# Performance work log

Hardware: AMD Instinct MI355X
Metric: run time of the kernel (lower is better)

## Reference

```python
import jax, jax.numpy as jnp
import numpy as np

N = 8192      # num nodes (pad index == N, matching the original's 15004 sentinel)
IN = 128; H = 128; OUT = 128
T = 512       # number of teams
L = 30        # max_len
SAMPLE = 5    # sample team size
DCAT = 2 * H + OUT


def _glorot(k, shape):
    lim = np.sqrt(6.0 / (shape[0] + shape[1]))
    return jax.random.uniform(k, shape, jnp.float32, -lim, lim)


def setup_inputs() -> dict:
    key = jax.random.key(0)
    ks = jax.random.split(key, 32)
    x = jax.random.normal(ks[0], (1, N, IN), jnp.float32)
    # sparse-ish binary dense adjacency, avg degree ~16 (memory-bound adj@x)
    adj = (jax.random.uniform(ks[1], (1, N, N), jnp.float32) < 16.0 / N).astype(jnp.float32)
    # team index matrix, ragged lengths in [SAMPLE+1, L], padded with N
    lens = jax.random.randint(ks[2], (T,), SAMPLE + 1, L + 1)
    ids = jax.random.randint(ks[3], (T, L), 0, N)
    teams = jnp.where(jnp.arange(L)[None, :] < lens[:, None], ids, N)
    # DenseGraphConv params: lin_rel (W,b) on adj@x, lin_root (no bias) on x
    p = dict(
        W1r=_glorot(ks[4], (IN, H)), b1=jnp.zeros((H,), jnp.float32), W1s=_glorot(ks[5], (IN, H)),
        W2r=_glorot(ks[6], (H, H)), b2=jnp.zeros((H,), jnp.float32), W2s=_glorot(ks[7], (H, H)),
        W3r=_glorot(ks[8], (H, OUT)), b3=jnp.zeros((OUT,), jnp.float32), W3s=_glorot(ks[9], (H, OUT)),
        g1=jnp.ones((H,), jnp.float32), be1=jnp.zeros((H,), jnp.float32),
        g2=jnp.ones((H,), jnp.float32), be2=jnp.zeros((H,), jnp.float32),
        g3=jnp.ones((OUT,), jnp.float32), be3=jnp.zeros((OUT,), jnp.float32),
        Wl=_glorot(ks[10], (DCAT, OUT)), bl=jnp.zeros((OUT,), jnp.float32),
        att=_glorot(ks[11], (T, L)),  # xavier_uniform'd attention vectors
    )
    return dict(x=x, adj=adj, teams=teams, sample_len=SAMPLE, **p)


def _bn(h, g, b):
    # BatchNorm1d in training mode over flattened (B*N, C), biased variance
    B, n, C = h.shape
    h2 = h.reshape(-1, C)
    mu = h2.mean(0)
    var = h2.var(0)
    return (((h2 - mu) * jax.lax.rsqrt(var + 1e-5)) * g + b).reshape(B, n, C)


def _conv(x, adj, Wr, br, Ws):
    # DenseGraphConv: lin_rel(adj @ x) + lin_root(x)
    return jnp.einsum('bnm,bmf,fo->bno', adj, x, Wr) + br + jnp.einsum('bnf,fo->bno', x, Ws)


def reference(x, adj, teams, sample_len, W1r, b1, W1s, W2r, b2, W2s, W3r, b3, W3s,
              g1, be1, g2, be2, g3, be3, Wl, bl, att):
    x1 = _bn(jax.nn.relu(_conv(x, adj, W1r, b1, W1s)), g1, be1)
    x2 = _bn(jax.nn.relu(_conv(x1, adj, W2r, b2, W2s)), g2, be2)
    x3 = _bn(jax.nn.relu(_conv(x2, adj, W3r, b3, W3s)), g3, be3)
    xcat = jnp.concatenate([x1, x2, x3], axis=-1)               # [1,N,DCAT]
    s = jax.nn.relu(xcat @ Wl + bl)
    appended = jnp.concatenate([xcat[0], jnp.zeros((1, xcat.shape[-1]), xcat.dtype)], 0)  # [N+1,D]
    gathered = appended[teams]                                   # [T,L,D] ragged gather
    # team: full softmax over attention vector (pad positions keep softmax mass,
    # but gather the zero row -> contribute zero, matching the original)
    a_team = jax.nn.softmax(att, axis=-1)
    team_emb = jnp.einsum('tl,tld->td', a_team, gathered)
    pos = jnp.arange(teams.shape[1])[None, :]
    # sample: sub-softmax over the attention entries at the sample members' positions
    m_s = pos < sample_len
    a_s = jax.nn.softmax(jnp.where(m_s, att, -1e30), axis=-1)
    sample_emb = jnp.einsum('tl,tld->td', a_s, gathered)
    # remain: team minus sample minus pad sentinel
    m_r = (pos >= sample_len) & (teams != N)
    a_r = jax.nn.softmax(jnp.where(m_r, att, -1e30), axis=-1)
    remain_emb = jnp.einsum('tl,tld->td', a_r, gathered)
    return s, xcat, team_emb, sample_emb, remain_emb
```

## Files before the change

### kernel.cpp

```cpp
#include <hip/hip_runtime.h>
#include <stdint.h>

#define NN 8192
#define CC 128
#define TT 512
#define LL 30
#define CAP 64

typedef unsigned int uint32;
typedef unsigned short u16;

typedef float f32x4 __attribute__((ext_vector_type(4)));
typedef short bf16x8 __attribute__((ext_vector_type(8)));

__device__ __forceinline__ float bf2f(uint32 h) { return __uint_as_float(h << 16); }
__device__ __forceinline__ u16 f2bf(float f) {
    uint32 u = __float_as_uint(f);
    u = (u + 0x7fffu + ((u >> 16) & 1u)) >> 16;
    return (u16)u;
}
__device__ __forceinline__ uint32 pack2(float a, float b) {
    return (uint32)f2bf(a) | ((uint32)f2bf(b) << 16);
}

__device__ __forceinline__ void stats_reduce(const float* __restrict__ P,
                                             const float* __restrict__ g,
                                             const float* __restrict__ be,
                                             float* __restrict__ coefOut, int tid) {
    __shared__ float SS[256], QQ[256];
    int c = tid & 127, half = tid >> 7;
    float s = 0.f, q = 0.f;
    int b0 = half * 128;
#pragma unroll 8
    for (int b = b0; b < b0 + 128; ++b) {
        s += P[b * 256 + c];
        q += P[b * 256 + 128 + c];
    }
    SS[tid] = s; QQ[tid] = q;
    __syncthreads();
    if (tid < 128) {
        float sum = SS[tid] + SS[tid + 128];
        float sq = QQ[tid] + QQ[tid + 128];
        float mu = sum * (1.f / NN);
        float var = sq * (1.f / NN) - mu * mu;
        float rs = rsqrtf(var + 1e-5f);
        float a = g[tid] * rs;
        coefOut[tid] = a;
        coefOut[128 + tid] = be[tid] - mu * a;
    }
}

__global__ __launch_bounds__(256) void k_pre(
    const float* __restrict__ adj,
    const float* __restrict__ W1r, const float* __restrict__ W1s,
    const float* __restrict__ W2r, const float* __restrict__ W2s,
    const float* __restrict__ W3r, const float* __restrict__ W3s,
    const float* __restrict__ Wl, const float* __restrict__ x0,
    int* __restrict__ nbr, int* __restrict__ cnt,
    u16* __restrict__ wfrag, u16* __restrict__ x0bf,
    u16* __restrict__ yp1, u16* __restrict__ yp2, u16* __restrict__ yp3,
    float* __restrict__ coefs) {
    int b = blockIdx.x, tid = threadIdx.x;
    if (b < 2048) {
        int row = b * 4 + (tid >> 6);
        int lane = tid & 63;
        const float4* arow = (const float4*)(adj + (size_t)row * NN);
        int base = 0;
        int* dst = nbr + (size_t)row * CAP;
        for (int it = 0; it < 32; ++it) {
            float4 v = arow[it * 64 + lane];
            float vv[4] = {v.x, v.y, v.z, v.w};
#pragma unroll
            for (int j = 0; j < 4; ++j) {
                unsigned long long m = __ballot(vv[j] != 0.f);
                if (vv[j] != 0.f) {
                    int pos = base + __popcll(m & ((1ull << lane) - 1ull));
                    if (pos < CAP) dst[pos] = it * 256 + lane * 4 + j;
                }
                base += __popcll(m);
            }
        }
        int nn = base < CAP ? base : CAP;
        int npad = (nn + 3) & ~3;
        for (int p = nn + lane; p < npad; p += 64) dst[p] = NN;
        if (lane == 0) cnt[row] = nn;
    } else if (b < 2336) {
        int bb = b - 2048;
        const float* Wa;
        const float* Wb;
        int tile, gbase;
        if (bb < 64)       { Wa = W1r; Wb = W1s; tile = bb;       gbase = 0; }
        else if (bb < 128) { Wa = W2r; Wb = W2s; tile = bb - 64;  gbase = 64; }
        else if (bb < 192) { Wa = W3r; Wb = W3s; tile = bb - 128; gbase = 128; }
        else               { Wa = Wl;  Wb = nullptr; tile = bb - 192; gbase = 192; }
        int kt = tile >> 3, nt = tile & 7;
        int lane = tid & 63, i0 = (tid >> 6) * 2;
        int n = nt * 16 + (lane & 15);
        u16* dst = wfrag + ((size_t)(gbase + tile) * 64 + lane) * 8;
#pragma unroll
        for (int ii = 0; ii < 2; ++ii) {
            int i = i0 + ii;
            int k = kt * 32 + ((lane >> 4) * 8) + i;
            float v;
            if (Wb) v = (k < 128) ? Wa[k * CC + n] : Wb[(k - 128) * CC + n];
            else    v = Wa[k * CC + n];
            dst[i] = f2bf(v);
        }
    } else if (b < 3360) {
        int idx = (b - 2336) * 1024 + tid * 4;
        float4 v = *(const float4*)(x0 + idx);
        ushort4 o;
        o.x = f2bf(v.x); o.y = f2bf(v.y); o.z = f2bf(v.z); o.w = f2bf(v.w);
        *(ushort4*)(x0bf + idx) = o;
    } else {
        if (tid < 128) {
            x0bf[(size_t)NN * CC + tid] = 0;
            yp1[(size_t)NN * CC + tid] = 0;
            yp2[(size_t)NN * CC + tid] = 0;
            yp3[(size_t)NN * CC + tid] = 0;
            coefs[tid] = 1.f;
            coefs[128 + tid] = 0.f;
        }
    }
}

__global__ __launch_bounds__(256) void k_agg(const u16* __restrict__ src,
                                             const int* __restrict__ nbr,
                                             const int* __restrict__ cnt,
                                             u16* __restrict__ Abraw,
                                             const float* __restrict__ P,
                                             const float* __restrict__ g,
                                             const float* __restrict__ be,
                                             float* __restrict__ coefOut) {
    if (blockIdx.x >= 2048) {
        stats_reduce(P, g, be, coefOut, threadIdx.x);
        return;
    }
    int row = blockIdx.x * 4 + (threadIdx.x >> 6);
    int lane = threadIdx.x & 63;
    int c = lane * 2;
    int nreal = cnt[row];
    int npad = (nreal + 3) & ~3;
    const int* nb = nbr + (size_t)row * CAP;
    float a0 = 0.f, a1 = 0.f;
    for (int j = 0; j < npad; j += 4) {
        int4 m = *(const int4*)(nb + j);
        uint32 v0 = *(const uint32*)(src + (size_t)m.x * CC + c);
        uint32 v1 = *(const uint32*)(src + (size_t)m.y * CC + c);
        uint32 v2 = *(const uint32*)(src + (size_t)m.z * CC + c);
        uint32 v3 = *(const uint32*)(src + (size_t)m.w * CC + c);
        a0 += bf2f(v0 & 0xffffu); a1 += bf2f(v0 >> 16);
        a0 += bf2f(v1 & 0xffffu); a1 += bf2f(v1 >> 16);
        a0 += bf2f(v2 & 0xffffu); a1 += bf2f(v2 >> 16);
        a0 += bf2f(v3 & 0xffffu); a1 += bf2f(v3 >> 16);
    }
    *(uint32*)(Abraw + (size_t)row * CC + c) = pack2(a0, a1);
}

__global__ __launch_bounds__(256) void k_gemm(const u16* __restrict__ Abraw,
                                              const u16* __restrict__ yprev,
                                              const int* __restrict__ cnt,
                                              const u16* __restrict__ wfrag,
                                              const float* __restrict__ bias,
                                              const float* __restrict__ coefIn,
                                              u16* __restrict__ yp,
                                              float* __restrict__ partials) {
    __shared__ u16 A[32][264];
    __shared__ float sSum[CC], sSq[CC];
    int tid = threadIdx.x, lane = tid & 63, wid = tid >> 6;
    int row0 = blockIdx.x * 32;
    if (tid < CC) { sSum[tid] = 0.f; sSq[tid] = 0.f; }
    for (int i = tid; i < 1024; i += 256) {
        int r = i >> 5, k = (i & 31) * 8;
        int row = row0 + r;
        uint4 raw;
        float fn;
        int c;
        if (k < 128) {
            c = k;
            raw = *(const uint4*)(Abraw + (size_t)row * CC + k);
            fn = (float)cnt[row];
        } else {
            c = k - 128;
            raw = *(const uint4*)(yprev + (size_t)row * CC + c);
            fn = 1.f;
        }
        float4 a0 = *(const float4*)(coefIn + c);
        float4 a1 = *(const float4*)(coefIn + c + 4);
        float4 b0 = *(const float4*)(coefIn + 128 + c);
        float4 b1 = *(const float4*)(coefIn + 128 + c + 4);
        uint4 o;
        o.x = pack2(a0.x * bf2f(raw.x & 0xffffu) + b0.x * fn, a0.y * bf2f(raw.x >> 16) + b0.y * fn);
        o.y = pack2(a0.z * bf2f(raw.y & 0xffffu) + b0.z * fn, a0.w * bf2f(raw.y >> 16) + b0.w * fn);
        o.z = pack2(a1.x * bf2f(raw.z & 0xffffu) + b1.x * fn, a1.y * bf2f(raw.z >> 16) + b1.y * fn);
        o.w = pack2(a1.z * bf2f(raw.w & 0xffffu) + b1.z * fn, a1.w * bf2f(raw.w >> 16) + b1.w * fn);
        *(uint4*)&A[r][k] = o;
    }
    __syncthreads();

    int mh = wid >> 1, nh = wid & 1;
    int arow = mh * 16 + (lane & 15);
    int kg = (lane >> 4) * 8;
    f32x4 acc[4];
#pragma unroll
    for (int nt = 0; nt < 4; ++nt) acc[nt] = (f32x4){0.f, 0.f, 0.f, 0.f};
#pragma unroll
    for (int kt = 0; kt < 8; ++kt) {
        bf16x8 a = *(const bf16x8*)&A[arow][kt * 32 + kg];
        const u16* wb = wfrag + ((size_t)(kt * 8 + nh * 4) * 64 + lane) * 8;
#pragma unroll
        for (int nt = 0; nt < 4; ++nt) {
            bf16x8 bfr = *(const bf16x8*)(wb + (size_t)nt * 512);
            acc[nt] = __builtin_amdgcn_mfma_f32_16x16x32_bf16(a, bfr, acc[nt], 0, 0, 0);
        }
    }
    int rowb = row0 + mh * 16 + ((lane >> 4) * 4);
#pragma unroll
    for (int nt = 0; nt < 4; ++nt) {
        int col = nh * 64 + nt * 16 + (lane & 15);
        float bv = bias[col];
        float s1 = 0.f, s2 = 0.f;
#pragma unroll
        for (int q = 0; q < 4; ++q) {
            float y = acc[nt][q] + bv;
            y = y > 0.f ? y : 0.f;
            yp[(size_t)(rowb + q) * CC + col] = f2bf(y);
            s1 += y;
            s2 += y * y;
        }
        s1 += __shfl_xor(s1, 16); s1 += __shfl_xor(s1, 32);
        s2 += __shfl_xor(s2, 16); s2 += __shfl_xor(s2, 32);
        if ((lane >> 4) == 0) { atomicAdd(&sSum[col], s1); atomicAdd(&sSq[col], s2); }
    }
    __syncthreads();
    if (tid < CC) {
        partials[(size_t)blockIdx.x * 256 + tid] = sSum[tid];
        partials[(size_t)blockIdx.x * 256 + CC + tid] = sSq[tid];
    }
}

__global__ __launch_bounds__(256) void k_coef3(const float* __restrict__ P,
                                               const float* __restrict__ g,
                                               const float* __restrict__ be,
                                               float* __restrict__ coefOut) {
    stats_reduce(P, g, be, coefOut, threadIdx.x);
}

__global__ __launch_bounds__(256) void k_gfinal(const u16* __restrict__ yp1,
                                                const u16* __restrict__ yp2,
                                                const u16* __restrict__ yp3,
                                                const float* __restrict__ coefs,
                                                const u16* __restrict__ wfrag,
                                                const float* __restrict__ bias,
                                                float* __restrict__ sout) {
    __shared__ u16 A[32][392];
    int tid = threadIdx.x, lane = tid & 63, wid = tid >> 6;
    int row0 = blockIdx.x * 32;
    for (int i = tid; i < 1536; i += 256) {
        int r = i / 48, kk = (i % 48) * 8;
        int seg = kk >> 7, c = kk & 127;
        const u16* sp = (seg == 0 ? yp1 : seg == 1 ? yp2 : yp3) + (size_t)(row0 + r) * CC + c;
        uint4 raw = *(const uint4*)sp;
        const float* cf = coefs + seg * 256;
        float4 av0 = *(const float4*)(cf + c);
        float4 av1 = *(const float4*)(cf + c + 4);
        float4 bv0 = *(const float4*)(cf + 128 + c);
        float4 bv1 = *(const float4*)(cf + 128 + c + 4);
        uint4 o;
        o.x = pack2(av0.x * bf2f(raw.x & 0xffffu) + bv0.x, av0.y * bf2f(raw.x >> 16) + bv0.y);
        o.y = pack2(av0.z * bf2f(raw.y & 0xffffu) + bv0.z, av0.w * bf2f(raw.y >> 16) + bv0.w);
        o.z = pack2(av1.x * bf2f(raw.z & 0xffffu) + bv1.x, av1.y * bf2f(raw.z >> 16) + bv1.y);
        o.w = pack2(av1.z * bf2f(raw.w & 0xffffu) + bv1.z, av1.w * bf2f(raw.w >> 16) + bv1.w);
        *(uint4*)&A[r][kk] = o;
    }
    __syncthreads();
    int mh = wid >> 1, nh = wid & 1;
    int arow = mh * 16 + (lane & 15);
    int kg = (lane >> 4) * 8;
    f32x4 acc[4];
#pragma unroll
    for (int nt = 0; nt < 4; ++nt) acc[nt] = (f32x4){0.f, 0.f, 0.f, 0.f};
#pragma unroll
    for (int kt = 0; kt < 12; ++kt) {
        bf16x8 a = *(const bf16x8*)&A[arow][kt * 32 + kg];
        const u16* wb = wfrag + ((size_t)(kt * 8 + nh * 4) * 64 + lane) * 8;
#pragma unroll
        for (int nt = 0; nt < 4; ++nt) {
            bf16x8 bfr = *(const bf16x8*)(wb + (size_t)nt * 512);
            acc[nt] = __builtin_amdgcn_mfma_f32_16x16x32_bf16(a, bfr, acc[nt], 0, 0, 0);
        }
    }
    int rowb = row0 + mh * 16 + ((lane >> 4) * 4);
#pragma unroll
    for (int nt = 0; nt < 4; ++nt) {
        int col = nh * 64 + nt * 16 + (lane & 15);
        float bv = bias[col];
#pragma unroll
        for (int q = 0; q < 4; ++q) {
            float y = acc[nt][q] + bv;
            sout[(size_t)(rowb + q) * CC + col] = y > 0.f ? y : 0.f;
        }
    }
}

__global__ __launch_bounds__(256) void k_tail(
    const u16* __restrict__ yp1, const u16* __restrict__ yp2, const u16* __restrict__ yp3,
    const float* __restrict__ coefs,
    const int* __restrict__ teams, const int* __restrict__ slen_p,
    const float* __restrict__ att,
    float* __restrict__ xcat,
    float* __restrict__ oT, float* __restrict__ oS, float* __restrict__ oR) {
    int b = blockIdx.x, tid = threadIdx.x;
    if (b < 512) {
        __shared__ float wT[LL], wS[LL], wR[LL];
        __shared__ int ids[LL];
        int t = b;
        if (tid < 64) {
            int lane = tid;
            bool act = lane < LL;
            float a = act ? att[t * LL + lane] : 0.f;
            int id = act ? teams[t * LL + lane] : NN;
            if (act) ids[lane] = id;
            int sl = *slen_p;
            const float NEG = -1e30f;
            float v = act ? a : NEG;
#pragma unroll
            for (int o = 32; o > 0; o >>= 1) v = fmaxf(v, __shfl_xor(v, o));
            float mT = v;
            float eT = act ? __expf(a - mT) : 0.f;
            v = eT;
#pragma unroll
            for (int o = 32; o > 0; o >>= 1) v += __shfl_xor(v, o);
            float sT = v;
            bool inS = act && (lane < sl);
            v = inS ? a : NEG;
#pragma unroll
            for (int o = 32; o > 0; o >>= 1) v = fmaxf(v, __shfl_xor(v, o));
            float mS = v;
            float eS = inS ? __expf(a - mS) : 0.f;
            v = eS;
#pragma unroll
            for (int o = 32; o > 0; o >>= 1) v += __shfl_xor(v, o);
            float sS = v;
            bool inR = act && (lane >= sl) && (id != NN);
            v = inR ? a : NEG;
#pragma unroll
            for (int o = 32; o > 0; o >>= 1) v = fmaxf(v, __shfl_xor(v, o));
            float mR = v;
            float eR = inR ? __expf(a - mR) : 0.f;
            v = eR;
#pragma unroll
            for (int o = 32; o > 0; o >>= 1) v += __shfl_xor(v, o);
            float sR = v;
            if (act) {
                wT[lane] = eT / sT;
                wS[lane] = eS / sS;
                wR[lane] = eR / sR;
            }
        }
        __syncthreads();
        for (int d = tid; d < 384; d += 256) {
            int seg = d >> 7, c = d & 127;
            const u16* xb = seg == 0 ? yp1 : seg == 1 ? yp2 : yp3;
            float ca = coefs[seg * 256 + c];
            float cb = coefs[seg * 256 + 128 + c];
            float aT = 0.f, aS = 0.f, aR = 0.f;
            for (int l = 0; l < LL; ++l) {
                int id = ids[l];
                if (id < NN) {
                    float vv = ca * bf2f((uint32)xb[(size_t)id * CC + c]) + cb;
                    aT += wT[l] * vv;
                    aS += wS[l] * vv;
                    aR += wR[l] * vv;
                }
            }
            oT[(size_t)t * 384 + d] = aT;
            oS[(size_t)t * 384 + d] = aS;
            oR[(size_t)t * 384 + d] = aR;
        }
    } else {
        int idx = (b - 512) * 256 + tid;
        int n = idx / 96;
        int k = (idx % 96) * 4;
        int seg = k >> 7, c = k & 127;
        const u16* sp = (seg == 0 ? yp1 : seg == 1 ? yp2 : yp3) + (size_t)n * CC + c;
        ushort4 raw = *(const ushort4*)sp;
        const float* cf = coefs + seg * 256;
        float4 a = *(const float4*)(cf + c);
        float4 bb = *(const float4*)(cf + 128 + c);
        float4 o;
        o.x = a.x * bf2f((uint32)raw.x) + bb.x;
        o.y = a.y * bf2f((uint32)raw.y) + bb.y;
        o.z = a.z * bf2f((uint32)raw.z) + bb.z;
        o.w = a.w * bf2f((uint32)raw.w) + bb.w;
        *(float4*)(xcat + (size_t)n * 384 + k) = o;
    }
}

extern "C" void kernel_launch(void* const* d_in, const int* in_sizes, int n_in,
                              void* d_out, int out_size, void* d_ws, size_t ws_size,
                              hipStream_t stream) {
    const float* x = (const float*)d_in[0];
    const float* adj = (const float*)d_in[1];
    const int* teams = (const int*)d_in[2];
    const int* slen = (const int*)d_in[3];
    const float* W1r = (const float*)d_in[4];
    const float* b1 = (const float*)d_in[5];
    const float* W1s = (const float*)d_in[6];
    const float* W2r = (const float*)d_in[7];
    const float* b2 = (const float*)d_in[8];
    const float* W2s = (const float*)d_in[9];
    const float* W3r = (const float*)d_in[10];
    const float* b3 = (const float*)d_in[11];
    const float* W3s = (const float*)d_in[12];
    const float* g1 = (const float*)d_in[13];
    const float* be1 = (const float*)d_in[14];
    const float* g2 = (const float*)d_in[15];
    const float* be2 = (const float*)d_in[16];
    const float* g3 = (const float*)d_in[17];
    const float* be3 = (const float*)d_in[18];
    const float* Wl = (const float*)d_in[19];
    const float* bl = (const float*)d_in[20];
    const float* att = (const float*)d_in[21];

    float* out = (float*)d_out;
    float* s_out = out;
    float* xcat = out + (size_t)NN * CC;
    float* oT = xcat + (size_t)NN * 384;
    float* oS = oT + (size_t)TT * 384;
    float* oR = oS + (size_t)TT * 384;

    char* ws = (char*)d_ws;
    size_t off = 0;
    int* nbr = (int*)(ws + off); off += (size_t)NN * CAP * 4;
    int* cnt = (int*)(ws + off); off += (size_t)NN * 4;
    u16* x0bf = (u16*)(ws + off); off += (size_t)(NN + 1) * CC * 2;
    u16* yp1 = (u16*)(ws + off); off += (size_t)(NN + 1) * CC * 2;
    u16* yp2 = (u16*)(ws + off); off += (size_t)(NN + 1) * CC * 2;
    u16* yp3 = (u16*)(ws + off); off += (size_t)(NN + 1) * CC * 2;
    u16* Abraw = (u16*)(ws + off); off += (size_t)NN * CC * 2;
    u16* wfrag = (u16*)(ws + off); off += (size_t)288 * 512 * 2;
    float* partials = (float*)(ws + off); off += (size_t)256 * 256 * 4;
    float* coefs = (float*)(ws + off); off += (size_t)4 * 256 * 4;

    k_pre<<<3361, 256, 0, stream>>>(adj, W1r, W1s, W2r, W2s, W3r, W3s, Wl, x,
                                    nbr, cnt, wfrag, x0bf, yp1, yp2, yp3, coefs);
    k_agg<<<2048, 256, 0, stream>>>(x0bf, nbr, cnt, Abraw, partials, g1, be1, coefs + 256);
    k_gemm<<<256, 256, 0, stream>>>(Abraw, x0bf, cnt, wfrag, b1, coefs, yp1, partials);
    k_agg<<<2049, 256, 0, stream>>>(yp1, nbr, cnt, Abraw, partials, g1, be1, coefs + 256);
    k_gemm<<<256, 256, 0, stream>>>(Abraw, yp1, cnt, wfrag + 64 * 512, b2, coefs + 256, yp2, partials);
    k_agg<<<2049, 256, 0, stream>>>(yp2, nbr, cnt, Abraw, partials, g2, be2, coefs + 512);
    k_gemm<<<256, 256, 0, stream>>>(Abraw, yp2, cnt, wfrag + 128 * 512, b3, coefs + 512, yp3, partials);
    k_coef3<<<1, 256, 0, stream>>>(partials, g3, be3, coefs + 768);
    k_gfinal<<<256, 256, 0, stream>>>(yp1, yp2, yp3, coefs + 256,
                                      wfrag + 192 * 512, bl, s_out);
    k_tail<<<3584, 256, 0, stream>>>(yp1, yp2, yp3, coefs + 256, teams, slen, att,
                                     xcat, oT, oS, oR);
}
```

Measured before the change: 137.6 us.

## Fuse final GEMM into tail kernel and widen layer GEMM blocks to 8 waves

Result: faster. 128.4 us (-6.6%).

```diff
diff --git a/kernel.cpp b/kernel.cpp
--- a/kernel.cpp
+++ b/kernel.cpp
@@ -157,7 +157,7 @@
     *(uint32*)(Abraw + (size_t)row * CC + c) = pack2(a0, a1);
 }
 
-__global__ __launch_bounds__(256) void k_gemm(const u16* __restrict__ Abraw,
+__global__ __launch_bounds__(512) void k_gemm(const u16* __restrict__ Abraw,
                                               const u16* __restrict__ yprev,
                                               const int* __restrict__ cnt,
                                               const u16* __restrict__ wfrag,
@@ -170,7 +170,7 @@
     int tid = threadIdx.x, lane = tid & 63, wid = tid >> 6;
     int row0 = blockIdx.x * 32;
     if (tid < CC) { sSum[tid] = 0.f; sSq[tid] = 0.f; }
-    for (int i = tid; i < 1024; i += 256) {
+    for (int i = tid; i < 1024; i += 512) {
         int r = i >> 5, k = (i & 31) * 8;
         int row = row0 + r;
         uint4 raw;
@@ -198,26 +198,26 @@
     }
     __syncthreads();
 
-    int mh = wid >> 1, nh = wid & 1;
+    int mh = wid >> 2, nh = wid & 3;
     int arow = mh * 16 + (lane & 15);
     int kg = (lane >> 4) * 8;
-    f32x4 acc[4];
-#pragma unroll
-    for (int nt = 0; nt < 4; ++nt) acc[nt] = (f32x4){0.f, 0.f, 0.f, 0.f};
+    f32x4 acc[2];
+#pragma unroll
+    for (int nt = 0; nt < 2; ++nt) acc[nt] = (f32x4){0.f, 0.f, 0.f, 0.f};
 #pragma unroll
     for (int kt = 0; kt < 8; ++kt) {
         bf16x8 a = *(const bf16x8*)&A[arow][kt * 32 + kg];
-        const u16* wb = wfrag + ((size_t)(kt * 8 + nh * 4) * 64 + lane) * 8;
-#pragma unroll
-        for (int nt = 0; nt < 4; ++nt) {
+        const u16* wb = wfrag + ((size_t)(kt * 8 + nh * 2) * 64 + lane) * 8;
+#pragma unroll
+        for (int nt = 0; nt < 2; ++nt) {
             bf16x8 bfr = *(const bf16x8*)(wb + (size_t)nt * 512);
             acc[nt] = __builtin_amdgcn_mfma_f32_16x16x32_bf16(a, bfr, acc[nt], 0, 0, 0);
         }
     }
     int rowb = row0 + mh * 16 + ((lane >> 4) * 4);
 #pragma unroll
-    for (int nt = 0; nt < 4; ++nt) {
-        int col = nh * 64 + nt * 16 + (lane & 15);
+    for (int nt = 0; nt < 2; ++nt) {
+        int col = nh * 32 + nt * 16 + (lane & 15);
         float bv = bias[col];
         float s1 = 0.f, s2 = 0.f;
 #pragma unroll
@@ -246,75 +246,68 @@
     stats_reduce(P, g, be, coefOut, threadIdx.x);
 }
 
-__global__ __launch_bounds__(256) void k_gfinal(const u16* __restrict__ yp1,
-                                                const u16* __restrict__ yp2,
-                                                const u16* __restrict__ yp3,
-                                                const float* __restrict__ coefs,
-                                                const u16* __restrict__ wfrag,
-                                                const float* __restrict__ bias,
-                                                float* __restrict__ sout) {
-    __shared__ u16 A[32][392];
-    int tid = threadIdx.x, lane = tid & 63, wid = tid >> 6;
-    int row0 = blockIdx.x * 32;
-    for (int i = tid; i < 1536; i += 256) {
-        int r = i / 48, kk = (i % 48) * 8;
-        int seg = kk >> 7, c = kk & 127;
-        const u16* sp = (seg == 0 ? yp1 : seg == 1 ? yp2 : yp3) + (size_t)(row0 + r) * CC + c;
-        uint4 raw = *(const uint4*)sp;
-        const float* cf = coefs + seg * 256;
-        float4 av0 = *(const float4*)(cf + c);
-        float4 av1 = *(const float4*)(cf + c + 4);
-        float4 bv0 = *(const float4*)(cf + 128 + c);
-        float4 bv1 = *(const float4*)(cf + 128 + c + 4);
-        uint4 o;
-        o.x = pack2(av0.x * bf2f(raw.x & 0xffffu) + bv0.x, av0.y * bf2f(raw.x >> 16) + bv0.y);
-        o.y = pack2(av0.z * bf2f(raw.y & 0xffffu) + bv0.z, av0.w * bf2f(raw.y >> 16) + bv0.w);
-        o.z = pack2(av1.x * bf2f(raw.z & 0xffffu) + bv1.x, av1.y * bf2f(raw.z >> 16) + bv1.y);
-        o.w = pack2(av1.z * bf2f(raw.w & 0xffffu) + bv1.z, av1.w * bf2f(raw.w >> 16) + bv1.w);
-        *(uint4*)&A[r][kk] = o;
-    }
-    __syncthreads();
-    int mh = wid >> 1, nh = wid & 1;
-    int arow = mh * 16 + (lane & 15);
-    int kg = (lane >> 4) * 8;
-    f32x4 acc[4];
-#pragma unroll
-    for (int nt = 0; nt < 4; ++nt) acc[nt] = (f32x4){0.f, 0.f, 0.f, 0.f};
-#pragma unroll
-    for (int kt = 0; kt < 12; ++kt) {
-        bf16x8 a = *(const bf16x8*)&A[arow][kt * 32 + kg];
-        const u16* wb = wfrag + ((size_t)(kt * 8 + nh * 4) * 64 + lane) * 8;
-#pragma unroll
-        for (int nt = 0; nt < 4; ++nt) {
-            bf16x8 bfr = *(const bf16x8*)(wb + (size_t)nt * 512);
-            acc[nt] = __builtin_amdgcn_mfma_f32_16x16x32_bf16(a, bfr, acc[nt], 0, 0, 0);
-        }
-    }
-    int rowb = row0 + mh * 16 + ((lane >> 4) * 4);
-#pragma unroll
-    for (int nt = 0; nt < 4; ++nt) {
-        int col = nh * 64 + nt * 16 + (lane & 15);
-        float bv = bias[col];
-#pragma unroll
-        for (int q = 0; q < 4; ++q) {
-            float y = acc[nt][q] + bv;
-            sout[(size_t)(rowb + q) * CC + col] = y > 0.f ? y : 0.f;
-        }
-    }
-}
-
-__global__ __launch_bounds__(256) void k_tail(
+__global__ __launch_bounds__(256) void k_out(
     const u16* __restrict__ yp1, const u16* __restrict__ yp2, const u16* __restrict__ yp3,
     const float* __restrict__ coefs,
+    const u16* __restrict__ wfrag, const float* __restrict__ bias,
     const int* __restrict__ teams, const int* __restrict__ slen_p,
     const float* __restrict__ att,
-    float* __restrict__ xcat,
+    float* __restrict__ sout, float* __restrict__ xcat,
     float* __restrict__ oT, float* __restrict__ oS, float* __restrict__ oR) {
     int b = blockIdx.x, tid = threadIdx.x;
     if (b < 512) {
+        __shared__ u16 A[16][392];
+        int lane = tid & 63, wid = tid >> 6;
+        int row0 = b * 16;
+        for (int i = tid; i < 768; i += 256) {
+            int r = i / 48, kk = (i % 48) * 8;
+            int seg = kk >> 7, c = kk & 127;
+            const u16* sp = (seg == 0 ? yp1 : seg == 1 ? yp2 : yp3) + (size_t)(row0 + r) * CC + c;
+            uint4 raw = *(const uint4*)sp;
+            const float* cf = coefs + seg * 256;
+            float4 av0 = *(const float4*)(cf + c);
+            float4 av1 = *(const float4*)(cf + c + 4);
+            float4 bv0 = *(const float4*)(cf + 128 + c);
+            float4 bv1 = *(const float4*)(cf + 128 + c + 4);
+            uint4 o;
+            o.x = pack2(av0.x * bf2f(raw.x & 0xffffu) + bv0.x, av0.y * bf2f(raw.x >> 16) + bv0.y);
+            o.y = pack2(av0.z * bf2f(raw.y & 0xffffu) + bv0.z, av0.w * bf2f(raw.y >> 16) + bv0.w);
+            o.z = pack2(av1.x * bf2f(raw.z & 0xffffu) + bv1.x, av1.y * bf2f(raw.z >> 16) + bv1.y);
+            o.w = pack2(av1.z * bf2f(raw.w & 0xffffu) + bv1.z, av1.w * bf2f(raw.w >> 16) + bv1.w);
+            *(uint4*)&A[r][kk] = o;
+        }
+        __syncthreads();
+        int nh = wid;
+        int arow = lane & 15;
+        int kg = (lane >> 4) * 8;
+        f32x4 acc[2];
+#pragma unroll
+        for (int nt = 0; nt < 2; ++nt) acc[nt] = (f32x4){0.f, 0.f, 0.f, 0.f};
+#pragma unroll
+        for (int kt = 0; kt < 12; ++kt) {
+            bf16x8 a = *(const bf16x8*)&A[arow][kt * 32 + kg];
+            const u16* wb = wfrag + ((size_t)(kt * 8 + nh * 2) * 64 + lane) * 8;
+#pragma unroll
+            for (int nt = 0; nt < 2; ++nt) {
+                bf16x8 bfr = *(const bf16x8*)(wb + (size_t)nt * 512);
+                acc[nt] = __builtin_amdgcn_mfma_f32_16x16x32_bf16(a, bfr, acc[nt], 0, 0, 0);
+            }
+        }
+        int rowb = row0 + ((lane >> 4) * 4);
+#pragma unroll
+        for (int nt = 0; nt < 2; ++nt) {
+            int col = nh * 32 + nt * 16 + (lane & 15);
+            float bv = bias[col];
+#pragma unroll
+            for (int q = 0; q < 4; ++q) {
+                float y = acc[nt][q] + bv;
+                sout[(size_t)(rowb + q) * CC + col] = y > 0.f ? y : 0.f;
+            }
+        }
+    } else if (b < 1024) {
         __shared__ float wT[LL], wS[LL], wR[LL];
         __shared__ int ids[LL];
-        int t = b;
+        int t = b - 512;
         if (tid < 64) {
             int lane = tid;
             bool act = lane < LL;
@@ -379,7 +372,7 @@
             oR[(size_t)t * 384 + d] = aR;
         }
     } else {
-        int idx = (b - 512) * 256 + tid;
+        int idx = (b - 1024) * 256 + tid;
         int n = idx / 96;
         int k = (idx % 96) * 4;
         int seg = k >> 7, c = k & 127;
@@ -446,14 +439,13 @@
     k_pre<<<3361, 256, 0, stream>>>(adj, W1r, W1s, W2r, W2s, W3r, W3s, Wl, x,
                                     nbr, cnt, wfrag, x0bf, yp1, yp2, yp3, coefs);
     k_agg<<<2048, 256, 0, stream>>>(x0bf, nbr, cnt, Abraw, partials, g1, be1, coefs + 256);
-    k_gemm<<<256, 256, 0, stream>>>(Abraw, x0bf, cnt, wfrag, b1, coefs, yp1, partials);
+    k_gemm<<<256, 512, 0, stream>>>(Abraw, x0bf, cnt, wfrag, b1, coefs, yp1, partials);
     k_agg<<<2049, 256, 0, stream>>>(yp1, nbr, cnt, Abraw, partials, g1, be1, coefs + 256);
-    k_gemm<<<256, 256, 0, stream>>>(Abraw, yp1, cnt, wfrag + 64 * 512, b2, coefs + 256, yp2, partials);
+    k_gemm<<<256, 512, 0, stream>>>(Abraw, yp1, cnt, wfrag + 64 * 512, b2, coefs + 256, yp2, partials);
     k_agg<<<2049, 256, 0, stream>>>(yp2, nbr, cnt, Abraw, partials, g2, be2, coefs + 512);
-    k_gemm<<<256, 256, 0, stream>>>(Abraw, yp2, cnt, wfrag + 128 * 512, b3, coefs + 512, yp3, partials);
+    k_gemm<<<256, 512, 0, stream>>>(Abraw, yp2, cnt, wfrag + 128 * 512, b3, coefs + 512, yp3, partials);
     k_coef3<<<1, 256, 0, stream>>>(partials, g3, be3, coefs + 768);
-    k_gfinal<<<256, 256, 0, stream>>>(yp1, yp2, yp3, coefs + 256,
-                                      wfrag + 192 * 512, bl, s_out);
-    k_tail<<<3584, 256, 0, stream>>>(yp1, yp2, yp3, coefs + 256, teams, slen, att,
-                                     xcat, oT, oS, oR);
-}
+    k_out<<<4096, 256, 0, stream>>>(yp1, yp2, yp3, coefs + 256,
+                                    wfrag + 192 * 512, bl, teams, slen, att,
+                                    s_out, xcat, oT, oS, oR);
+}
```
